# Optimization experiments

Measured on AMD Instinct MI355X. Metric: run time of the kernel, lower is better.

Reference implementation:

```python
import jax, jax.numpy as jnp
import numpy as np
import math

H = 1024
N = 64          # d_state; complex modes = N // 2
N2 = N // 2
B = 8
L = 2048
DT_MIN, DT_MAX = 0.001, 0.1


def setup_inputs() -> dict:
    key = jax.random.key(0)
    ks = jax.random.split(key, 8)
    u = jax.random.normal(ks[0], (B, H, L), dtype=jnp.float32)
    # log_dt ~ Uniform[log(dt_min), log(dt_max)]
    log_dt = (jax.random.uniform(ks[1], (H,), dtype=jnp.float32)
              * (math.log(DT_MAX) - math.log(DT_MIN)) + math.log(DT_MIN))
    # random_dplr with scaling='inverse': real part 0.5, imag = (1/pi)*N*(N/(1+2n)-1)
    n = jnp.arange(N2, dtype=jnp.float32)
    w_real = 0.5 * jnp.ones((1, N2), dtype=jnp.float32)
    w_imag = ((1.0 / math.pi) * N * (N / (1.0 + 2.0 * n) - 1.0))[None, :].astype(jnp.float32)
    log_w_real = jnp.log(w_real + 1e-4)  # module stores log(-w.real + 1e-4)
    # C = randn complex (channels=1, H, N2), scaled by normalized B (folded into randn here)
    C_re = jax.random.normal(ks[2], (1, H, N2), dtype=jnp.float32) / math.sqrt(2 * N2)
    C_im = jax.random.normal(ks[3], (1, H, N2), dtype=jnp.float32) / math.sqrt(2 * N2)
    D = jax.random.normal(ks[4], (1, H), dtype=jnp.float32)
    # output_linear: Conv1d(k=1) from channels*H -> H  => weight (H, H)
    W_out = jax.random.normal(ks[5], (H, H), dtype=jnp.float32) / math.sqrt(H)
    b_out = jax.random.normal(ks[6], (H,), dtype=jnp.float32) * 0.01
    return {"u": u, "log_dt": log_dt, "log_w_real": log_w_real, "w_imag": w_imag,
            "C_re": C_re, "C_im": C_im, "D": D, "W_out": W_out, "b_out": b_out}


def reference(u, log_dt, log_w_real, w_imag, C_re, C_im, D, W_out, b_out):
    b, h, l = u.shape
    # --- SSKernelDiag.forward ---
    dt = jnp.exp(log_dt)                                   # (H,)
    w = -jnp.exp(log_w_real) + 1j * w_imag                 # (n_ssm=1, N2)
    w = jnp.broadcast_to(w, (h, w.shape[-1]))              # repeat copies -> (H, N2)
    dtA = w * dt[:, None]                                  # (H, N2) complex
    C = (C_re + 1j * C_im) * (jnp.exp(dtA) - 1.0) / w      # (c, H, N2)
    # Vandermonde: exp(dtA * arange(L)) -> (H, N2, L) complex
    K = jnp.exp(dtA[:, :, None] * jnp.arange(l, dtype=jnp.float32))
    k = 2.0 * jnp.einsum('chn,hnl->chl', C, K).real        # (c, H, L) float
    # --- FFT convolution ---
    k_f = jnp.fft.rfft(k, n=2 * l)                         # (c, H, L+1)
    u_f = jnp.fft.rfft(u, n=2 * l)                         # (B, H, L+1)
    y_f = jnp.einsum('bhl,chl->bchl', u_f, k_f)
    y = jnp.fft.irfft(y_f, n=2 * l)[..., :l]               # (B, c, H, L)
    # skip connection with D
    y = y + jnp.einsum('bhl,ch->bchl', u, D)
    y = y.reshape(b, -1, l)                                # (B, c*H, L)
    y = jax.nn.gelu(y, approximate=False)
    # output 1x1 conv: (B, c*H, L) x (H, c*H) -> (B, H, L)
    y = jnp.einsum('bil,oi->bol', y, W_out) + b_out[None, :, None]
    return y
```

## Files before the change

### kernel.cpp

```cpp
#include <hip/hip_runtime.h>
#include <hip/hip_bf16.h>

#define HH 1024
#define LL 2048
#define BB 8
#define NN2 32
#define CT 128
#define NCH 16

typedef short bf16x8 __attribute__((ext_vector_type(8)));
typedef float f32x4  __attribute__((ext_vector_type(4)));

static __device__ __forceinline__ unsigned short bfbits(float x) {
    __hip_bfloat16 h = __float2bfloat16(x);
    return *(unsigned short*)&h;
}
static __device__ __forceinline__ float f_from_bits(unsigned short b) {
    __hip_bfloat16 h; *(unsigned short*)&h = b; return __bfloat162float(h);
}
static __device__ __forceinline__ float2 cexp_n(float2 dA, float p) {
    float mag = __expf(dA.x * p);
    float rev = dA.y * p * 0.15915494309f;
    rev -= floorf(rev);
    float ang = rev * 6.28318530718f;
    return make_float2(mag * __cosf(ang), mag * __sinf(ang));
}
static __device__ __forceinline__ float gelu_f(float y) {
    float z = 0.7978845608f * (y + 0.044715f * y * y * y);
    float e = __expf(2.0f * z);
    return 0.5f * y * (1.0f + (1.0f - 2.0f / (e + 1.0f)));
}

#define SWZ(off, row) ((off) ^ (((row) & 7) << 4))

__global__ __launch_bounds__(256) void aux_tables(
    const float* __restrict__ log_dt, const float* __restrict__ log_w_real,
    const float* __restrict__ w_imag, const float* __restrict__ C_re,
    const float* __restrict__ C_im, const float* __restrict__ W,
    __hip_bfloat16* __restrict__ AJ_g, __hip_bfloat16* __restrict__ AP_g,
    float* __restrict__ misc_g, __hip_bfloat16* __restrict__ Wb)
{
    __shared__ float2 dtA_s[NN2];
    __shared__ float2 Cn_s[NN2];
    const int tid = threadIdx.x;
    const int h = blockIdx.x;

    {
        float4 v = ((const float4*)(W + (size_t)h * HH))[tid];
        ushort4 o;
        o.x = bfbits(v.x); o.y = bfbits(v.y); o.z = bfbits(v.z); o.w = bfbits(v.w);
        ((ushort4*)(Wb + (size_t)h * HH))[tid] = o;
    }

    if (tid < NN2) {
        int n = tid;
        float dt = expf(log_dt[h]);
        float wr = -expf(log_w_real[n]);
        float wi = w_imag[n];
        float dar = wr * dt, dai = wi * dt;
        dtA_s[n] = make_float2(dar, dai);
        float er = expf(dar);
        float sn, cs; sincosf(dai, &sn, &cs);
        float exr = er * cs - 1.0f, exi = er * sn;
        float den = wr * wr + wi * wi;
        float fr = (exr * wr + exi * wi) / den;
        float fi = (exi * wr - exr * wi) / den;
        float cre = C_re[h * NN2 + n], cim = C_im[h * NN2 + n];
        float2 Cv = make_float2(cre * fr - cim * fi, cre * fi + cim * fr);
        Cn_s[n] = Cv;
        misc_g[h * 256 + 128 + 2 * n]     = Cv.x;
        misc_g[h * 256 + 128 + 2 * n + 1] = Cv.y;
        float magA = expf(dar * 128.0f);
        float snA, csA; sincosf(dai * 128.0f, &snA, &csA);
        misc_g[h * 256 + 192 + 2 * n]     = magA * csA;
        misc_g[h * 256 + 192 + 2 * n + 1] = magA * snA;
    }
    __syncthreads();

    char* ajb = (char*)AJ_g + (size_t)h * 16384;
    #pragma unroll
    for (int q = 0; q < 2; ++q) {
        int task = q * 256 + tid;
        int n = task >> 4, j0 = (task & 15) * 8;
        float2 dA = dtA_s[n];
        unsigned rw[4], iw[4];
        #pragma unroll
        for (int i2 = 0; i2 < 4; ++i2) {
            float2 a0 = cexp_n(dA, (float)(127 - j0 - 2 * i2));
            float2 a1 = cexp_n(dA, (float)(127 - j0 - 2 * i2 - 1));
            rw[i2] = (unsigned)bfbits(a0.x) | ((unsigned)bfbits(a1.x) << 16);
            iw[i2] = (unsigned)bfbits(a0.y) | ((unsigned)bfbits(a1.y) << 16);
        }
        int r0 = 2 * n, r1 = 2 * n + 1;
        *(uint4*)(ajb + SWZ(r0 * 256 + j0 * 2, r0)) = make_uint4(rw[0], rw[1], rw[2], rw[3]);
        *(uint4*)(ajb + SWZ(r1 * 256 + j0 * 2, r1)) = make_uint4(iw[0], iw[1], iw[2], iw[3]);
    }

    char* apb = (char*)AP_g + (size_t)h * 16384;
    #pragma unroll
    for (int q = 0; q < 2; ++q) {
        int task = q * 256 + tid;
        int ttr = task >> 2, n0 = (task & 3) * 8;
        unsigned w[8];
        #pragma unroll
        for (int i = 0; i < 8; ++i) {
            float2 a = cexp_n(dtA_s[n0 + i], (float)(ttr + 1));
            w[i] = (unsigned)bfbits(2.0f * a.x) | ((unsigned)bfbits(-2.0f * a.y) << 16);
        }
        *(uint4*)(apb + SWZ(ttr * 128 + n0 * 4, ttr))      = make_uint4(w[0], w[1], w[2], w[3]);
        *(uint4*)(apb + SWZ(ttr * 128 + n0 * 4 + 16, ttr)) = make_uint4(w[4], w[5], w[6], w[7]);
    }

    {
        int t = tid >> 1, nb = (tid & 1) * 16;
        float s = 0.f;
        #pragma unroll
        for (int i = 0; i < 16; ++i) {
            int n = nb + i;
            float2 a = cexp_n(dtA_s[n], (float)t);
            float2 C = Cn_s[n];
            s += C.x * a.x - C.y * a.y;
        }
        s += __shfl_xor(s, 1);
        if ((tid & 1) == 0) misc_g[h * 256 + t] = 2.0f * s;
    }
}

#define S_U    0
#define S_UN   16384
#define S_P    32768
#define S_KT   40960
#define S_KTP  41984
#define S_TOT  46208

__global__ __launch_bounds__(512, 6) void ssm_mfma(
    const float* __restrict__ u,
    const __hip_bfloat16* __restrict__ AJ_g,
    const __hip_bfloat16* __restrict__ AP_g,
    const float* __restrict__ misc_g,
    const float* __restrict__ Dp, __hip_bfloat16* __restrict__ g_out)
{
    extern __shared__ char smem[];
    float*  kt   = (float*)(smem + S_KT);
    float2* CnL  = (float2*)(smem + S_KT + 512);
    float2* A128 = (float2*)(smem + S_KT + 768);

    const int tid  = threadIdx.x;
    const int lane = tid & 63;
    const int wave = tid >> 6;
    const int wm   = wave >> 2;
    const int wn   = wave & 3;
    const int h    = blockIdx.x;
    const int bh   = blockIdx.y;

    {
        const char* ajs = (const char*)AJ_g + (size_t)h * 16384;
        __builtin_amdgcn_global_load_lds(
            (const __attribute__((address_space(1))) void*)(ajs + tid * 16),
            (__attribute__((address_space(3))) void*)(smem + S_UN + wave * 1024), 16, 0, 0);
        __builtin_amdgcn_global_load_lds(
            (const __attribute__((address_space(1))) void*)(ajs + 8192 + tid * 16),
            (__attribute__((address_space(3))) void*)(smem + S_UN + 8192 + wave * 1024), 16, 0, 0);
        if (tid < 64) {
            const char* ms = (const char*)misc_g + (size_t)h * 1024;
            __builtin_amdgcn_global_load_lds(
                (const __attribute__((address_space(1))) void*)(ms + tid * 16),
                (__attribute__((address_space(3))) void*)(smem + S_KT), 16, 0, 0);
        }
    }

    float4 ureg[4];
    #pragma unroll
    for (int q = 0; q < 4; ++q) {
        int b = bh * 4 + q;
        ureg[q] = *(const float4*)(u + ((size_t)(b * HH + h)) * LL + tid * 4);
    }
    #pragma unroll
    for (int q = 0; q < 4; ++q) {
        int row = q * 16 + (tid >> 5);
        int j   = (tid & 31) * 4;
        ushort4 o;
        o.x = bfbits(ureg[q].x); o.y = bfbits(ureg[q].y);
        o.z = bfbits(ureg[q].z); o.w = bfbits(ureg[q].w);
        *(ushort4*)(smem + SWZ(S_U + row * 256 + j * 2, row)) = o;
    }
    asm volatile("s_waitcnt vmcnt(0)" ::: "memory");
    __syncthreads();

    {
        int s = wave;
        int i0 = lane * 4;
        ushort4 o;
        #pragma unroll
        for (int k = 0; k < 4; ++k) {
            int src = 127 - s - (i0 + k);
            ((unsigned short*)&o)[k] = (src >= 0) ? bfbits(kt[src]) : (unsigned short)0;
        }
        *(ushort4*)(smem + S_KTP + s * 528 + i0 * 2) = o;
        if (lane < 2) {
            *(ushort4*)(smem + S_KTP + s * 528 + 512 + lane * 8) = make_ushort4(0, 0, 0, 0);
        }
    }

    f32x4 accP[2] = {};
    #pragma unroll
    for (int ks = 0; ks < 4; ++ks) {
        int kf = ks * 32 + (lane >> 4) * 8;
        bf16x8 a0, a1, b0;
        {
            int r = wm * 32 + (lane & 15);
            a0 = *(bf16x8*)(smem + SWZ(S_U + r * 256 + kf * 2, r));
            int r2 = r + 16;
            a1 = *(bf16x8*)(smem + SWZ(S_U + r2 * 256 + kf * 2, r2));
        }
        {
            int r = wn * 16 + (lane & 15);
            b0 = *(bf16x8*)(smem + SWZ(S_UN + r * 256 + kf * 2, r));
        }
        accP[0] = __builtin_amdgcn_mfma_f32_16x16x32_bf16(a0, b0, accP[0], 0, 0, 0);
        accP[1] = __builtin_amdgcn_mfma_f32_16x16x32_bf16(a1, b0, accP[1], 0, 0, 0);
    }
    #pragma unroll
    for (int mt = 0; mt < 2; ++mt)
        #pragma unroll
        for (int r = 0; r < 4; ++r) {
            int row = wm * 32 + mt * 16 + (lane >> 4) * 4 + r;
            int col = wn * 16 + (lane & 15);
            *(unsigned short*)(smem + SWZ(S_P + row * 128 + col * 2, row)) =
                bfbits(accP[mt][r]);
        }
    __syncthreads();

    {
        const char* aps = (const char*)AP_g + (size_t)h * 16384;
        __builtin_amdgcn_global_load_lds(
            (const __attribute__((address_space(1))) void*)(aps + tid * 16),
            (__attribute__((address_space(3))) void*)(smem + S_UN + wave * 1024), 16, 0, 0);
        __builtin_amdgcn_global_load_lds(
            (const __attribute__((address_space(1))) void*)(aps + 8192 + tid * 16),
            (__attribute__((address_space(3))) void*)(smem + S_UN + 8192 + wave * 1024), 16, 0, 0);
    }

    if (tid < 128) {
        int b = tid >> 5, n = tid & 31;
        float2 C = CnL[n];
        float2 A = A128[n];
        unsigned int pv[NCH];
        int offs[NCH];
        #pragma unroll
        for (int c = 0; c < NCH; ++c) {
            int row = b * 16 + c;
            offs[c] = SWZ(S_P + row * 128 + n * 4, row);
            pv[c] = *(unsigned int*)(smem + offs[c]);
        }
        float sr = 0.f, si = 0.f;
        #pragma unroll
        for (int c = 0; c < NCH; ++c) {
            float pr = f_from_bits((unsigned short)(pv[c] & 0xffff));
            float pi = f_from_bits((unsigned short)(pv[c] >> 16));
            float csr = C.x * sr - C.y * si;
            float csi = C.x * si + C.y * sr;
            *(unsigned int*)(smem + offs[c]) =
                (unsigned)bfbits(csr) | ((unsigned)bfbits(csi) << 16);
            float nsr = A.x * sr - A.y * si + pr;
            float nsi = A.x * si + A.y * sr + pi;
            sr = nsr; si = nsi;
        }
    }

    f32x4 acc[2][2] = {};
    #pragma unroll
    for (int ks = 0; ks < 4; ++ks) {
        int kf = ks * 32 + (lane >> 4) * 8;
        bf16x8 a0, a1, bv[2];
        {
            int r = wm * 32 + (lane & 15);
            a0 = *(bf16x8*)(smem + SWZ(S_U + r * 256 + kf * 2, r));
            int r2 = r + 16;
            a1 = *(bf16x8*)(smem + SWZ(S_U + r2 * 256 + kf * 2, r2));
        }
        #pragma unroll
        for (int nt = 0; nt < 2; ++nt) {
            int ttr = wn * 32 + nt * 16 + (lane & 15);
            int s   = (127 - ttr) & 7;
            int gq  = (127 - ttr + kf) >> 3;
            bv[nt] = *(bf16x8*)(smem + S_KTP + s * 528 + gq * 16);
        }
        #pragma unroll
        for (int nt = 0; nt < 2; ++nt) {
            acc[0][nt] = __builtin_amdgcn_mfma_f32_16x16x32_bf16(a0, bv[nt], acc[0][nt], 0, 0, 0);
            acc[1][nt] = __builtin_amdgcn_mfma_f32_16x16x32_bf16(a1, bv[nt], acc[1][nt], 0, 0, 0);
        }
    }
    asm volatile("s_waitcnt vmcnt(0)" ::: "memory");
    __syncthreads();

    #pragma unroll
    for (int ks = 0; ks < 2; ++ks) {
        int kf = ks * 32 + (lane >> 4) * 8;
        bf16x8 a0, a1, bv[2];
        {
            int r = wm * 32 + (lane & 15);
            a0 = *(bf16x8*)(smem + SWZ(S_P + r * 128 + kf * 2, r));
            int r2 = r + 16;
            a1 = *(bf16x8*)(smem + SWZ(S_P + r2 * 128 + kf * 2, r2));
        }
        #pragma unroll
        for (int nt = 0; nt < 2; ++nt) {
            int ttr = wn * 32 + nt * 16 + (lane & 15);
            bv[nt] = *(bf16x8*)(smem + SWZ(S_UN + ttr * 128 + kf * 2, ttr));
        }
        #pragma unroll
        for (int nt = 0; nt < 2; ++nt) {
            acc[0][nt] = __builtin_amdgcn_mfma_f32_16x16x32_bf16(a0, bv[nt], acc[0][nt], 0, 0, 0);
            acc[1][nt] = __builtin_amdgcn_mfma_f32_16x16x32_bf16(a1, bv[nt], acc[1][nt], 0, 0, 0);
        }
    }

    const float Dv = Dp[h];
    #pragma unroll
    for (int mt = 0; mt < 2; ++mt)
        #pragma unroll
        for (int nt = 0; nt < 2; ++nt)
            #pragma unroll
            for (int r = 0; r < 4; ++r) {
                int row = wm * 32 + mt * 16 + (lane >> 4) * 4 + r;
                int ttr = wn * 32 + nt * 16 + (lane & 15);
                int off = SWZ(S_U + row * 256 + ttr * 2, row);
                float uv = f_from_bits(*(unsigned short*)(smem + off));
                float y = acc[mt][nt][r] + Dv * uv;
                *(unsigned short*)(smem + off) = bfbits(y);
            }
    __syncthreads();
    #pragma unroll
    for (int q = 0; q < 2; ++q) {
        int flat = q * 512 + tid;
        int row = flat >> 4, c16 = flat & 15;
        uint4 v = *(uint4*)(smem + SWZ(S_U + row * 256 + c16 * 16, row));
        int b = bh * 4 + (row >> 4), c = row & 15;
        *(uint4*)(g_out + ((size_t)(b * HH + h)) * LL + c * CT + c16 * 8) = v;
    }
}

__global__ __launch_bounds__(256) void transpose_g(
    const __hip_bfloat16* __restrict__ g, __hip_bfloat16* __restrict__ gT)
{
    __shared__ __hip_bfloat16 t[64][66];
    const int tid = threadIdx.x;
    const int b  = blockIdx.z;
    const int h0 = blockIdx.x * 64;
    const int l0 = blockIdx.y * 64;

    #pragma unroll
    for (int q = 0; q < 2; ++q) {
        int idx = tid + q * 256;
        int r = idx >> 3, c8 = (idx & 7) * 8;
        uint4 v = *(const uint4*)(g + ((size_t)(b * HH + h0 + r)) * LL + l0 + c8);
        unsigned int* dst = (unsigned int*)&t[r][c8];
        unsigned int* src = (unsigned int*)&v;
        #pragma unroll
        for (int w = 0; w < 4; ++w) {
            unsigned int pw = src[w];
            float a = gelu_f(f_from_bits((unsigned short)(pw & 0xffff)));
            float c = gelu_f(f_from_bits((unsigned short)(pw >> 16)));
            dst[w] = (unsigned)bfbits(a) | ((unsigned)bfbits(c) << 16);
        }
    }
    __syncthreads();
    #pragma unroll
    for (int q = 0; q < 2; ++q) {
        int idx = tid + q * 256;
        int r = idx >> 3, c8 = (idx & 7) * 8;
        unsigned short tmp[8];
        #pragma unroll
        for (int j = 0; j < 8; ++j) tmp[j] = *(unsigned short*)&t[c8 + j][r];
        uint4 o;
        o.x = (unsigned)tmp[0] | ((unsigned)tmp[1] << 16);
        o.y = (unsigned)tmp[2] | ((unsigned)tmp[3] << 16);
        o.z = (unsigned)tmp[4] | ((unsigned)tmp[5] << 16);
        o.w = (unsigned)tmp[6] | ((unsigned)tmp[7] << 16);
        *(uint4*)(gT + ((size_t)(b * LL + l0 + r)) * HH + h0 + c8) = o;
    }
}

#define QSLOT 65536

#define STAGE_A_HALF(kt_, s_, h_)                                                \
    {                                                                            \
        const int k0_ = (kt_) * 64;                                              \
        _Pragma("unroll")                                                        \
        for (int v2_ = 0; v2_ < 2; ++v2_) {                                      \
            int v_ = (h_) * 2 + v2_;                                             \
            int row_ = v_ * 64 + rsub;                                           \
            const __hip_bfloat16* ga_ = Wb + (size_t)(o0 + row_) * HH + k0_ + csw; \
            char* dA_ = smem + (s_) * QSLOT + (v_ * 64 + wave * 8) * 128;        \
            __builtin_amdgcn_global_load_lds(                                    \
                (const __attribute__((address_space(1))) void*)ga_,              \
                (__attribute__((address_space(3))) void*)dA_, 16, 0, 0);         \
        }                                                                        \
    }

#define STAGE_B_HALF(kt_, s_, h_)                                                \
    {                                                                            \
        const int k0_ = (kt_) * 64;                                              \
        _Pragma("unroll")                                                        \
        for (int v2_ = 0; v2_ < 2; ++v2_) {                                      \
            int v_ = (h_) * 2 + v2_;                                             \
            int row_ = v_ * 64 + rsub;                                           \
            const __hip_bfloat16* gb_ = gT + (size_t)(n0 + row_) * HH + k0_ + csw; \
            char* dB_ = smem + (s_) * QSLOT + 32768 + (v_ * 64 + wave * 8) * 128; \
            __builtin_amdgcn_global_load_lds(                                    \
                (const __attribute__((address_space(1))) void*)gb_,              \
                (__attribute__((address_space(3))) void*)dB_, 16, 0, 0);         \
        }                                                                        \
    }

#define READ_A(af_, qa_)                                                         \
    _Pragma("unroll")                                                            \
    for (int mt = 0; mt < 2; ++mt)                                               \
        _Pragma("unroll")                                                        \
        for (int ks = 0; ks < 2; ++ks) {                                         \
            int ra = (qa_) * 128 + wm4 * 32 + mt * 16 + (lane & 15);             \
            int c  = (ks * 32 + (lane >> 4) * 8) ^ ((ra & 7) << 3);              \
            af_[mt][ks] = *(const bf16x8*)(baseA + ra * 128 + c * 2);            \
        }

#define READ_B(bf_, qb_)                                                         \
    _Pragma("unroll")                                                            \
    for (int nt = 0; nt < 4; ++nt)                                               \
        _Pragma("unroll")                                                        \
        for (int ks = 0; ks < 2; ++ks) {                                         \
            int rb = (qb_) * 128 + wn2 * 64 + nt * 16 + (lane & 15);             \
            int c  = (ks * 32 + (lane >> 4) * 8) ^ ((rb & 7) << 3);              \
            bf_[nt][ks] = *(const bf16x8*)(baseB + rb * 128 + c * 2);            \
        }

#define DO_MFMA(qa_, qb_, af_, bf_)                                              \
    _Pragma("unroll")                                                            \
    for (int mt = 0; mt < 2; ++mt)                                               \
        _Pragma("unroll")                                                        \
        for (int nt = 0; nt < 4; ++nt) {                                         \
            acc[qa_][qb_][mt][nt] = __builtin_amdgcn_mfma_f32_16x16x32_bf16(     \
                af_[mt][0], bf_[nt][0], acc[qa_][qb_][mt][nt], 0, 0, 0);         \
            acc[qa_][qb_][mt][nt] = __builtin_amdgcn_mfma_f32_16x16x32_bf16(     \
                af_[mt][1], bf_[nt][1], acc[qa_][qb_][mt][nt], 0, 0, 0);         \
        }

#define TILE_BODY(t_, s_, W0, W1, W2, DOSTAGE)                                   \
    {                                                                            \
        const char* baseA = smem + (s_) * QSLOT;                                 \
        const char* baseB = smem + (s_) * QSLOT + 32768;                         \
        bf16x8 af0[2][2], af1[2][2], bf[4][2];                                   \
                                                    \
        asm volatile("s_waitcnt vmcnt(" #W0 ")" ::: "memory");                   \
        __builtin_amdgcn_s_barrier();                                            \
        if (DOSTAGE) STAGE_A_HALF((t_) + 1, (s_) ^ 1, 0)                         \
        READ_A(af0, 0)                                                           \
        READ_B(bf, 0)                                                            \
        DO_MFMA(0, 0, af0, bf)                                                   \
                                                    \
        asm volatile("s_waitcnt vmcnt(" #W1 ")" ::: "memory");                   \
        __builtin_amdgcn_s_barrier();                                            \
        if (DOSTAGE) STAGE_B_HALF((t_) + 1, (s_) ^ 1, 0)                         \
        READ_A(af1, 1)                                                           \
        DO_MFMA(1, 0, af1, bf)                                                   \
                                                    \
        asm volatile("s_waitcnt vmcnt(" #W2 ")" ::: "memory");                   \
        __builtin_amdgcn_s_barrier();                                            \
        if (DOSTAGE) STAGE_A_HALF((t_) + 1, (s_) ^ 1, 1)                         \
        READ_B(bf, 1)                                                            \
        DO_MFMA(1, 1, af1, bf)                                                   \
              \
        if (DOSTAGE) STAGE_B_HALF((t_) + 1, (s_) ^ 1, 1)                         \
        DO_MFMA(0, 1, af0, bf)                                                   \
    }

__global__ __launch_bounds__(512) void out_gemm_256p(
    const __hip_bfloat16* __restrict__ Wb,
    const __hip_bfloat16* __restrict__ gT,
    const float* __restrict__ bias,
    float* __restrict__ out)
{
    extern __shared__ char smem[];
    const int tid  = threadIdx.x;
    const int lane = tid & 63;
    const int wave = tid >> 6;
    const int wm4 = wave >> 1;
    const int wn2 = wave & 1;

    int wg  = blockIdx.x;
    int swz = (wg & 7) * 32 + (wg >> 3);
    const int o0 = (swz & 3) * 256;
    const int n0 = (swz >> 2) * 256;

    const int rsub = tid >> 3;
    const int csw  = ((tid & 7) ^ (rsub & 7)) << 3;

    f32x4 acc[2][2][2][4] = {};

    STAGE_A_HALF(0, 0, 0)
    STAGE_B_HALF(0, 0, 0)
    STAGE_A_HALF(0, 0, 1)
    STAGE_B_HALF(0, 0, 1)

    for (int t = 0; t < 15; ++t) {
        TILE_BODY(t, (t & 1), 4, 4, 4, 1)
    }
    TILE_BODY(15, 1, 4, 2, 0, 0)

    const int bb  = n0 >> 11;
    const int l0g = n0 & 2047;
    #pragma unroll
    for (int qa = 0; qa < 2; ++qa)
        #pragma unroll
        for (int mt = 0; mt < 2; ++mt)
            #pragma unroll
            for (int r = 0; r < 4; ++r) {
                int o = o0 + qa * 128 + wm4 * 32 + mt * 16 + (lane >> 4) * 4 + r;
                float bo = bias[o];
                #pragma unroll
                for (int qb = 0; qb < 2; ++qb)
                    #pragma unroll
                    for (int nt = 0; nt < 4; ++nt) {
                        int l = l0g + qb * 128 + wn2 * 64 + nt * 16 + (lane & 15);
                        out[((size_t)(bb * HH + o)) * LL + l] =
                            acc[qa][qb][mt][nt][r] + bo;
                    }
            }
}

extern "C" void kernel_launch(void* const* d_in, const int* in_sizes, int n_in,
                              void* d_out, int out_size, void* d_ws, size_t ws_size,
                              hipStream_t stream) {
    const float* u          = (const float*)d_in[0];
    const float* log_dt     = (const float*)d_in[1];
    const float* log_w_real = (const float*)d_in[2];
    const float* w_imag     = (const float*)d_in[3];
    const float* C_re       = (const float*)d_in[4];
    const float* C_im       = (const float*)d_in[5];
    const float* Dp         = (const float*)d_in[6];
    const float* W          = (const float*)d_in[7];
    const float* bias       = (const float*)d_in[8];
    float* out = (float*)d_out;

    __hip_bfloat16* AJ_g = (__hip_bfloat16*)d_out;
    __hip_bfloat16* AP_g = (__hip_bfloat16*)((char*)d_out + 16777216);
    __hip_bfloat16* g    = (__hip_bfloat16*)((char*)d_out + 33554432);
    __hip_bfloat16* gT     = (__hip_bfloat16*)d_ws;
    __hip_bfloat16* Wb     = (__hip_bfloat16*)((char*)d_ws + 33554432);
    float*          misc_g = (float*)((char*)d_ws + 35651584);

    hipFuncSetAttribute((const void*)ssm_mfma,
                        hipFuncAttributeMaxDynamicSharedMemorySize, S_TOT);
    hipFuncSetAttribute((const void*)out_gemm_256p,
                        hipFuncAttributeMaxDynamicSharedMemorySize, 131072);

    aux_tables<<<dim3(HH), 256, 0, stream>>>(log_dt, log_w_real, w_imag,
                                             C_re, C_im, W, AJ_g, AP_g, misc_g, Wb);
    ssm_mfma<<<dim3(HH, 2), 512, S_TOT, stream>>>(u, AJ_g, AP_g, misc_g, Dp, g);
    transpose_g<<<dim3(HH / 64, LL / 64, BB), 256, 0, stream>>>(g, gT);
    out_gemm_256p<<<dim3(256), 512, 131072, stream>>>(Wb, gT, bias, out);
}
```

Baseline: 96.19 us.

## Compute AP powers table in-kernel instead of loading from global; add MFMA setprio

The per-channel AP table (2*exp(dtA*(t+1)), 16KB per channel) is no longer precomputed by aux_tables and loaded via global_load_lds. ssm_mfma now loads dtA from the misc buffer and generates the table directly into shared memory. This removes 16MB of global writes plus reads, at the cost of extra transcendental work in each of the 2048 blocks. The output GEMM also wraps its MFMA groups with s_setprio to favour matrix issue over other waves.

New measurement: 93.82 us. 2.5% less time.

```diff
diff --git a/kernel.cpp b/kernel.cpp
--- a/kernel.cpp
+++ b/kernel.cpp
@@ -37,8 +37,8 @@
     const float* __restrict__ log_dt, const float* __restrict__ log_w_real,
     const float* __restrict__ w_imag, const float* __restrict__ C_re,
     const float* __restrict__ C_im, const float* __restrict__ W,
-    __hip_bfloat16* __restrict__ AJ_g, __hip_bfloat16* __restrict__ AP_g,
-    float* __restrict__ misc_g, __hip_bfloat16* __restrict__ Wb)
+    __hip_bfloat16* __restrict__ AJ_g, float* __restrict__ misc_g,
+    __hip_bfloat16* __restrict__ Wb)
 {
     __shared__ float2 dtA_s[NN2];
     __shared__ float2 Cn_s[NN2];
@@ -68,12 +68,14 @@
         float cre = C_re[h * NN2 + n], cim = C_im[h * NN2 + n];
         float2 Cv = make_float2(cre * fr - cim * fi, cre * fi + cim * fr);
         Cn_s[n] = Cv;
-        misc_g[h * 256 + 128 + 2 * n]     = Cv.x;
-        misc_g[h * 256 + 128 + 2 * n + 1] = Cv.y;
+        misc_g[h * 384 + 128 + 2 * n]     = Cv.x;
+        misc_g[h * 384 + 128 + 2 * n + 1] = Cv.y;
         float magA = expf(dar * 128.0f);
         float snA, csA; sincosf(dai * 128.0f, &snA, &csA);
-        misc_g[h * 256 + 192 + 2 * n]     = magA * csA;
-        misc_g[h * 256 + 192 + 2 * n + 1] = magA * snA;
+        misc_g[h * 384 + 192 + 2 * n]     = magA * csA;
+        misc_g[h * 384 + 192 + 2 * n + 1] = magA * snA;
+        misc_g[h * 384 + 256 + 2 * n]     = dar;
+        misc_g[h * 384 + 256 + 2 * n + 1] = dai;
     }
     __syncthreads();
 
@@ -96,21 +98,6 @@
         *(uint4*)(ajb + SWZ(r1 * 256 + j0 * 2, r1)) = make_uint4(iw[0], iw[1], iw[2], iw[3]);
     }
 
-    char* apb = (char*)AP_g + (size_t)h * 16384;
-    #pragma unroll
-    for (int q = 0; q < 2; ++q) {
-        int task = q * 256 + tid;
-        int ttr = task >> 2, n0 = (task & 3) * 8;
-        unsigned w[8];
-        #pragma unroll
-        for (int i = 0; i < 8; ++i) {
-            float2 a = cexp_n(dtA_s[n0 + i], (float)(ttr + 1));
-            w[i] = (unsigned)bfbits(2.0f * a.x) | ((unsigned)bfbits(-2.0f * a.y) << 16);
-        }
-        *(uint4*)(apb + SWZ(ttr * 128 + n0 * 4, ttr))      = make_uint4(w[0], w[1], w[2], w[3]);
-        *(uint4*)(apb + SWZ(ttr * 128 + n0 * 4 + 16, ttr)) = make_uint4(w[4], w[5], w[6], w[7]);
-    }
-
     {
         int t = tid >> 1, nb = (tid & 1) * 16;
         float s = 0.f;
@@ -122,7 +109,7 @@
             s += C.x * a.x - C.y * a.y;
         }
         s += __shfl_xor(s, 1);
-        if ((tid & 1) == 0) misc_g[h * 256 + t] = 2.0f * s;
+        if ((tid & 1) == 0) misc_g[h * 384 + t] = 2.0f * s;
     }
 }
 
@@ -130,13 +117,12 @@
 #define S_UN   16384
 #define S_P    32768
 #define S_KT   40960
-#define S_KTP  41984
-#define S_TOT  46208
+#define S_KTP  42496
+#define S_TOT  46720
 
 __global__ __launch_bounds__(512, 6) void ssm_mfma(
     const float* __restrict__ u,
     const __hip_bfloat16* __restrict__ AJ_g,
-    const __hip_bfloat16* __restrict__ AP_g,
     const float* __restrict__ misc_g,
     const float* __restrict__ Dp, __hip_bfloat16* __restrict__ g_out)
 {
@@ -144,6 +130,7 @@
     float*  kt   = (float*)(smem + S_KT);
     float2* CnL  = (float2*)(smem + S_KT + 512);
     float2* A128 = (float2*)(smem + S_KT + 768);
+    float2* dtAL = (float2*)(smem + S_KT + 1024);
 
     const int tid  = threadIdx.x;
     const int lane = tid & 63;
@@ -161,11 +148,15 @@
         __builtin_amdgcn_global_load_lds(
             (const __attribute__((address_space(1))) void*)(ajs + 8192 + tid * 16),
             (__attribute__((address_space(3))) void*)(smem + S_UN + 8192 + wave * 1024), 16, 0, 0);
+        const char* ms = (const char*)misc_g + (size_t)h * 1536;
         if (tid < 64) {
-            const char* ms = (const char*)misc_g + (size_t)h * 1024;
             __builtin_amdgcn_global_load_lds(
                 (const __attribute__((address_space(1))) void*)(ms + tid * 16),
                 (__attribute__((address_space(3))) void*)(smem + S_KT), 16, 0, 0);
+        } else if (tid < 96) {
+            __builtin_amdgcn_global_load_lds(
+                (const __attribute__((address_space(1))) void*)(ms + tid * 16),
+                (__attribute__((address_space(3))) void*)(smem + S_KT + 1024), 16, 0, 0);
         }
     }
 
@@ -231,14 +222,14 @@
         }
     __syncthreads();
 
-    {
-        const char* aps = (const char*)AP_g + (size_t)h * 16384;
-        __builtin_amdgcn_global_load_lds(
-            (const __attribute__((address_space(1))) void*)(aps + tid * 16),
-            (__attribute__((address_space(3))) void*)(smem + S_UN + wave * 1024), 16, 0, 0);
-        __builtin_amdgcn_global_load_lds(
-            (const __attribute__((address_space(1))) void*)(aps + 8192 + tid * 16),
-            (__attribute__((address_space(3))) void*)(smem + S_UN + 8192 + wave * 1024), 16, 0, 0);
+    #pragma unroll
+    for (int q = 0; q < 8; ++q) {
+        int idx = q * 512 + tid;
+        int n = idx >> 7, ttr = idx & 127;
+        float2 a = cexp_n(dtAL[n], (float)(ttr + 1));
+        int off = SWZ(S_UN + ttr * 128 + n * 4, ttr);
+        *(unsigned int*)(smem + off) =
+            (unsigned)bfbits(2.0f * a.x) | ((unsigned)bfbits(-2.0f * a.y) << 16);
     }
 
     if (tid < 128) {
@@ -292,7 +283,6 @@
             acc[1][nt] = __builtin_amdgcn_mfma_f32_16x16x32_bf16(a1, bv[nt], acc[1][nt], 0, 0, 0);
         }
     }
-    asm volatile("s_waitcnt vmcnt(0)" ::: "memory");
     __syncthreads();
 
     #pragma unroll
@@ -436,6 +426,7 @@
         }
 
 #define DO_MFMA(qa_, qb_, af_, bf_)                                              \
+    __builtin_amdgcn_s_setprio(1);                                               \
     _Pragma("unroll")                                                            \
     for (int mt = 0; mt < 2; ++mt)                                               \
         _Pragma("unroll")                                                        \
@@ -444,33 +435,30 @@
                 af_[mt][0], bf_[nt][0], acc[qa_][qb_][mt][nt], 0, 0, 0);         \
             acc[qa_][qb_][mt][nt] = __builtin_amdgcn_mfma_f32_16x16x32_bf16(     \
                 af_[mt][1], bf_[nt][1], acc[qa_][qb_][mt][nt], 0, 0, 0);         \
-        }
+        }                                                                        \
+    __builtin_amdgcn_s_setprio(0);
 
 #define TILE_BODY(t_, s_, W0, W1, W2, DOSTAGE)                                   \
     {                                                                            \
         const char* baseA = smem + (s_) * QSLOT;                                 \
         const char* baseB = smem + (s_) * QSLOT + 32768;                         \
         bf16x8 af0[2][2], af1[2][2], bf[4][2];                                   \
-                                                    \
         asm volatile("s_waitcnt vmcnt(" #W0 ")" ::: "memory");                   \
         __builtin_amdgcn_s_barrier();                                            \
         if (DOSTAGE) STAGE_A_HALF((t_) + 1, (s_) ^ 1, 0)                         \
         READ_A(af0, 0)                                                           \
-        READ_B(bf, 0)                                                            \
+        READ_B(bf, 0)                                                           \
         DO_MFMA(0, 0, af0, bf)                                                   \
-                                                    \
         asm volatile("s_waitcnt vmcnt(" #W1 ")" ::: "memory");                   \
         __builtin_amdgcn_s_barrier();                                            \
         if (DOSTAGE) STAGE_B_HALF((t_) + 1, (s_) ^ 1, 0)                         \
         READ_A(af1, 1)                                                           \
         DO_MFMA(1, 0, af1, bf)                                                   \
-                                                    \
         asm volatile("s_waitcnt vmcnt(" #W2 ")" ::: "memory");                   \
         __builtin_amdgcn_s_barrier();                                            \
         if (DOSTAGE) STAGE_A_HALF((t_) + 1, (s_) ^ 1, 1)                         \
-        READ_B(bf, 1)                                                            \
+        READ_B(bf, 1)                                                           \
         DO_MFMA(1, 1, af1, bf)                                                   \
-              \
         if (DOSTAGE) STAGE_B_HALF((t_) + 1, (s_) ^ 1, 1)                         \
         DO_MFMA(0, 1, af0, bf)                                                   \
     }
@@ -543,12 +531,11 @@
     const float* bias       = (const float*)d_in[8];
     float* out = (float*)d_out;
 
-    __hip_bfloat16* AJ_g = (__hip_bfloat16*)d_out;
-    __hip_bfloat16* AP_g = (__hip_bfloat16*)((char*)d_out + 16777216);
-    __hip_bfloat16* g    = (__hip_bfloat16*)((char*)d_out + 33554432);
-    __hip_bfloat16* gT     = (__hip_bfloat16*)d_ws;
-    __hip_bfloat16* Wb     = (__hip_bfloat16*)((char*)d_ws + 33554432);
-    float*          misc_g = (float*)((char*)d_ws + 35651584);
+    __hip_bfloat16* AJ_g   = (__hip_bfloat16*)d_out;
+    float*          misc_g = (float*)((char*)d_out + 16777216);
+    __hip_bfloat16* g      = (__hip_bfloat16*)((char*)d_out + 33554432);
+    __hip_bfloat16* gT = (__hip_bfloat16*)d_ws;
+    __hip_bfloat16* Wb = (__hip_bfloat16*)((char*)d_ws + 33554432);
 
     hipFuncSetAttribute((const void*)ssm_mfma,
                         hipFuncAttributeMaxDynamicSharedMemorySize, S_TOT);
@@ -556,8 +543,8 @@
                         hipFuncAttributeMaxDynamicSharedMemorySize, 131072);
 
     aux_tables<<<dim3(HH), 256, 0, stream>>>(log_dt, log_w_real, w_imag,
-                                             C_re, C_im, W, AJ_g, AP_g, misc_g, Wb);
-    ssm_mfma<<<dim3(HH, 2), 512, S_TOT, stream>>>(u, AJ_g, AP_g, misc_g, Dp, g);
+                                             C_re, C_im, W, AJ_g, misc_g, Wb);
+    ssm_mfma<<<dim3(HH, 2), 512, S_TOT, stream>>>(u, AJ_g, misc_g, Dp, g);
     transpose_g<<<dim3(HH / 64, LL / 64, BB), 256, 0, stream>>>(g, gT);
     out_gemm_256p<<<dim3(256), 512, 131072, stream>>>(Wb, gT, bias, out);
 }
```
